# Kernel tuning notes

Measured on AMD Instinct MI355X. Metric: run time of the kernel, lower is better.

## Reference

```python
import jax, jax.numpy as jnp
import numpy as np
from jax import lax

B, L, D, DM, S, M, P = 8, 2048, 512, 1024, 32, 4, 4096


def setup_inputs() -> dict:
    key = jax.random.key(0)
    ks = jax.random.split(key, 13)
    emb = jax.random.normal(ks[0], (B, L, D), jnp.float32)
    pos = jax.random.randint(ks[1], (B, L), 1, P + 1)          # pos >= 1 (0 reserved for CLS)
    sid = jax.random.randint(ks[2], (B, L), 0, S)
    mod = jax.random.randint(ks[3], (B, L), 0, M)
    role = jax.random.randint(ks[4], (B, L), 0, 3)
    padding_mask = jax.random.uniform(ks[5], (B, L)) < 0.9
    W_proj = jax.random.normal(ks[6], (S, DM, D), jnp.float32) / np.float32(np.sqrt(D))
    b_proj = jax.random.normal(ks[7], (S, DM), jnp.float32) * 0.01
    cls_content = jax.random.normal(ks[8], (DM,), jnp.float32)
    pos_emb = jax.random.normal(ks[9], (P + 1, DM), jnp.float32) * 0.02
    id_emb = jax.random.normal(ks[10], (S + 1, DM), jnp.float32) * 0.02
    mod_emb = jax.random.normal(ks[11], (M, DM), jnp.float32) * 0.02
    role_emb = jax.random.normal(ks[12], (3, DM), jnp.float32) * 0.02
    return dict(emb=emb, pos=pos, sid=sid, mod=mod, role=role, padding_mask=padding_mask,
                W_proj=W_proj, b_proj=b_proj, cls_content=cls_content,
                pos_emb=pos_emb, id_emb=id_emb, mod_emb=mod_emb, role_emb=role_emb)


def _moe_project(emb, sid, padding_mask, W_proj, b_proj):
    """Per-token per-signal Linear: tokens[b,l] = W_proj[sid[b,l]] @ emb[b,l] + b_proj[sid[b,l]].
    Computed as S dense GEMMs masked per token (dense-dispatch MoE), avoiding an
    O(B*L*DM*D) gathered-weight tensor."""
    def step(acc, sWb):
        s, W, b = sWb
        y = jnp.einsum('bld,od->blo', emb, W) + b  # (B, L, DM)
        m = (sid == s) & padding_mask              # padded tokens stay zero
        return acc + jnp.where(m[..., None], y, 0.0), None
    acc0 = jnp.zeros(emb.shape[:2] + (W_proj.shape[1],), emb.dtype)
    acc, _ = lax.scan(step, acc0, (jnp.arange(W_proj.shape[0]), W_proj, b_proj))
    return acc


def reference(emb, pos, sid, mod, role, padding_mask,
              W_proj, b_proj, cls_content, pos_emb, id_emb, mod_emb, role_emb):
    Bc, Lc = pos.shape
    dm = cls_content.shape[0]
    cls_id = id_emb.shape[0] - 1  # == num_signals

    proj = _moe_project(emb, sid, padding_mask, W_proj, b_proj)  # (B, L, DM)

    cls = jnp.broadcast_to(cls_content, (Bc, 1, dm))
    tokens = jnp.concatenate([cls, proj], axis=1)                # (B, L+1, DM)

    pos_full = jnp.concatenate([jnp.zeros((Bc, 1), pos.dtype), pos], axis=1)
    sid_full = jnp.concatenate([jnp.full((Bc, 1), cls_id, sid.dtype), sid], axis=1)
    tokens = tokens + pos_emb[pos_full] + id_emb[sid_full]

    # modality + role embeddings only on non-CLS tokens (added even where padded, as in torch)
    tokens = tokens.at[:, 1:, :].add(mod_emb[mod] + role_emb[role])

    attn_keep = jnp.concatenate([jnp.ones((Bc, 1), bool), padding_mask], axis=1)
    return tokens, attn_keep
```

## Files before the change

### kernel.cpp

```cpp
#include <hip/hip_runtime.h>
#include <hip/hip_bf16.h>


#define NB   8
#define NL   2048
#define ND   512
#define NDM  1024
#define NS   32
#define NTOK (NB * NL)
#define LP1  (NL + 1)
#define MAXTILES 160
#define EXP_CAP 1024

static __device__ __forceinline__ size_t attn_off() { return (size_t)NB * LP1 * NDM; }

typedef __attribute__((ext_vector_type(8))) short bf16x8;
typedef __attribute__((ext_vector_type(4))) float f32x4;

__device__ __forceinline__ unsigned short f2bf(float f) {
    unsigned int x = __float_as_uint(f);
    x += 0x7fffu + ((x >> 16) & 1u);
    return (unsigned short)(x >> 16);
}

__device__ __forceinline__ float bf2f(unsigned short s) {
    return __uint_as_float(((unsigned int)s) << 16);
}

__device__ __forceinline__ bf16x8 cvt8(float4 a, float4 b) {
    bf16x8 r;
    r[0] = (short)__bfloat16_as_ushort(__float2bfloat16(a.x));
    r[1] = (short)__bfloat16_as_ushort(__float2bfloat16(a.y));
    r[2] = (short)__bfloat16_as_ushort(__float2bfloat16(a.z));
    r[3] = (short)__bfloat16_as_ushort(__float2bfloat16(a.w));
    r[4] = (short)__bfloat16_as_ushort(__float2bfloat16(b.x));
    r[5] = (short)__bfloat16_as_ushort(__float2bfloat16(b.y));
    r[6] = (short)__bfloat16_as_ushort(__float2bfloat16(b.z));
    r[7] = (short)__bfloat16_as_ushort(__float2bfloat16(b.w));
    return r;
}

__device__ __forceinline__ float4 ld4(const float* p) { return *(const float4*)p; }
__device__ __forceinline__ float4 add4(float4 a, float4 b) {
    return make_float4(a.x + b.x, a.y + b.y, a.z + b.z, a.w + b.w);
}

__global__ void k_bucket(const int* __restrict__ sid, const int* __restrict__ mask,
                         int* __restrict__ cnt, int* __restrict__ kidx,
                         int* __restrict__ tokList, float* __restrict__ out) {
    int t = blockIdx.x * 256 + threadIdx.x;
    if (t >= NTOK) return;
    int s = sid[t];
    bool keep = mask[t] != 0;
    int b = t >> 11, l = t & (NL - 1);
    out[attn_off() + (size_t)b * LP1 + l + 1] = keep ? 1.0f : 0.0f;
    if (t < NB) out[attn_off() + (size_t)t * LP1] = 1.0f;
    int ki = -1;
    if (keep) {
        ki = atomicAdd(&cnt[s], 1);
        if (ki < EXP_CAP) tokList[s * EXP_CAP + ki] = t;
    }
    kidx[t] = ki;
}

__global__ void k_tiles(const int* __restrict__ cnt, int* __restrict__ meta,
                        int* __restrict__ bOff, int4* __restrict__ tiles,
                        const float* __restrict__ me, const float* __restrict__ re,
                        float* __restrict__ mrT) {
    if (threadIdx.x == 0) {
        int idx = 0, cbase = 0;
        for (int e = 0; e < NS; ++e) {
            int c = min(cnt[e], EXP_CAP);
            bOff[e] = cbase;
            for (int r = 0; r < c; r += 128)
                tiles[idx++] = make_int4(e, r, min(128, c - r), cbase + r);
            cbase += c;
        }
        meta[0] = idx;
    }
    for (int i = threadIdx.x; i < 12 * (NDM / 4); i += 256) {
        int mr = i / (NDM / 4); int o = (i % (NDM / 4)) * 4;
        int m = mr / 3, ro = mr % 3;
        float4 v = add4(ld4(me + (size_t)m * NDM + o), ld4(re + (size_t)ro * NDM + o));
        *(float4*)&mrT[(size_t)mr * NDM + o] = v;
    }
}

__global__ __launch_bounds__(256, 4) void k_gemm(
    const float* __restrict__ emb, const float* __restrict__ Wp,
    const int* __restrict__ tokList, const int4* __restrict__ tiles,
    const int* __restrict__ meta, unsigned short* __restrict__ projC) {
    if (blockIdx.x >= meta[0]) return;
    int4 td = tiles[blockIdx.x];
    const int e = td.x, rowBase = td.y, nRows = td.z, cBase = td.w;
    const int nBase = blockIdx.y * 128;

    __shared__ short SA[128 * 32];
    __shared__ short SB[128 * 32];

    const int tid  = threadIdx.x;
    const int lane = tid & 63;
    const int w    = tid >> 6;
    const int wr   = w >> 1, wc = w & 1;
    const int fr   = lane & 15, kg = lane >> 4;

    const int srow = tid >> 2;
    const int sch  = tid & 3;
    const size_t eBase = (size_t)e * EXP_CAP + rowBase;
    int ar0 = (srow < nRows) ? srow : 0;
    int ar1 = (srow + 64 < nRows) ? srow + 64 : 0;
    int tok0 = tokList[eBase + ar0];
    int tok1 = tokList[eBase + ar1];
    const float* a0 = emb + (size_t)tok0 * ND + sch * 8;
    const float* a1 = emb + (size_t)tok1 * ND + sch * 8;
    const float* b0 = Wp + ((size_t)e * NDM + nBase + srow) * ND + sch * 8;
    const float* b1 = Wp + ((size_t)e * NDM + nBase + srow + 64) * ND + sch * 8;
    const int wo0 = srow * 32 + (sch ^ ((srow >> 1) & 3)) * 8;
    const int wo1 = wo0 + 64 * 32;

    f32x4 acc[4][4];
#pragma unroll
    for (int i = 0; i < 4; ++i)
#pragma unroll
        for (int j = 0; j < 4; ++j)
            acc[i][j] = (f32x4){0.f, 0.f, 0.f, 0.f};

    float4 ra0a = ld4(a0), ra0b = ld4(a0 + 4);
    float4 ra1a = ld4(a1), ra1b = ld4(a1 + 4);
    float4 rb0a = ld4(b0), rb0b = ld4(b0 + 4);
    float4 rb1a = ld4(b1), rb1b = ld4(b1 + 4);

    const int pc = kg ^ ((fr >> 1) & 3);
    for (int ks = 0; ks < ND / 32; ++ks) {
        __syncthreads();
        *(bf16x8*)&SA[wo0] = cvt8(ra0a, ra0b);
        *(bf16x8*)&SA[wo1] = cvt8(ra1a, ra1b);
        *(bf16x8*)&SB[wo0] = cvt8(rb0a, rb0b);
        *(bf16x8*)&SB[wo1] = cvt8(rb1a, rb1b);
        __syncthreads();
        if (ks < ND / 32 - 1) {
            const float* na0 = a0 + (ks + 1) * 32;
            const float* na1 = a1 + (ks + 1) * 32;
            const float* nb0 = b0 + (ks + 1) * 32;
            const float* nb1 = b1 + (ks + 1) * 32;
            ra0a = ld4(na0); ra0b = ld4(na0 + 4);
            ra1a = ld4(na1); ra1b = ld4(na1 + 4);
            rb0a = ld4(nb0); rb0b = ld4(nb0 + 4);
            rb1a = ld4(nb1); rb1b = ld4(nb1 + 4);
        }
        bf16x8 af[4], bv[4];
#pragma unroll
        for (int i = 0; i < 4; ++i)
            af[i] = *(const bf16x8*)&SA[(wr * 64 + i * 16 + fr) * 32 + pc * 8];
#pragma unroll
        for (int j = 0; j < 4; ++j)
            bv[j] = *(const bf16x8*)&SB[(wc * 64 + j * 16 + fr) * 32 + pc * 8];
#pragma unroll
        for (int i = 0; i < 4; ++i)
#pragma unroll
            for (int j = 0; j < 4; ++j)
                acc[i][j] = __builtin_amdgcn_mfma_f32_16x16x32_bf16(af[i], bv[j], acc[i][j], 0, 0, 0);
    }

#pragma unroll
    for (int i = 0; i < 4; ++i) {
#pragma unroll
        for (int r = 0; r < 4; ++r) {
            int row = wr * 64 + i * 16 + kg * 4 + r;
            if (row < nRows) {
                size_t crow = (size_t)(cBase + row) * NDM + nBase;
#pragma unroll
                for (int j = 0; j < 4; ++j)
                    projC[crow + wc * 64 + j * 16 + fr] = f2bf(acc[i][j][r]);
            }
        }
    }
}

__global__ void k_out(const int* __restrict__ pos, const int* __restrict__ sid,
                      const int* __restrict__ mod, const int* __restrict__ role,
                      const int* __restrict__ mask, const int* __restrict__ kidx,
                      const int* __restrict__ bOff,
                      const float* __restrict__ bp, const float* __restrict__ cls_c,
                      const float* __restrict__ pe, const float* __restrict__ ie,
                      const float* __restrict__ mrT,
                      const unsigned short* __restrict__ projC,
                      float* __restrict__ out) {
    int l1 = blockIdx.x;
    int b  = blockIdx.y;
    int o  = threadIdx.x * 4;
    float4 v;
    if (l1 == 0) {
        v = add4(add4(ld4(cls_c + o), ld4(pe + o)), ld4(ie + (size_t)NS * NDM + o));
    } else {
        int t = b * NL + l1 - 1;
        int p = pos[t], s = sid[t], mr = mod[t] * 3 + role[t];
        v = add4(ld4(pe + (size_t)p * NDM + o), ld4(ie + (size_t)s * NDM + o));
        v = add4(v, ld4(mrT + (size_t)mr * NDM + o));
        if (mask[t] != 0) {
            v = add4(v, ld4(bp + (size_t)s * NDM + o));
            int ki = kidx[t];
            if (ki >= 0 && ki < EXP_CAP) {
                const unsigned short* pr = projC + (size_t)(bOff[s] + ki) * NDM + o;
                v.x += bf2f(pr[0]); v.y += bf2f(pr[1]);
                v.z += bf2f(pr[2]); v.w += bf2f(pr[3]);
            }
        }
    }
    *(float4*)&out[((size_t)b * LP1 + l1) * NDM + o] = v;
}

extern "C" void kernel_launch(void* const* d_in, const int* in_sizes, int n_in,
                              void* d_out, int out_size, void* d_ws, size_t ws_size,
                              hipStream_t stream) {
    const float* emb  = (const float*)d_in[0];
    const int* pos    = (const int*)d_in[1];
    const int* sid    = (const int*)d_in[2];
    const int* mod    = (const int*)d_in[3];
    const int* role   = (const int*)d_in[4];
    const int* mask   = (const int*)d_in[5];
    const float* Wp   = (const float*)d_in[6];
    const float* bp   = (const float*)d_in[7];
    const float* cls  = (const float*)d_in[8];
    const float* pe   = (const float*)d_in[9];
    const float* ie   = (const float*)d_in[10];
    const float* me   = (const float*)d_in[11];
    const float* re   = (const float*)d_in[12];
    float* out = (float*)d_out;

    int* ws        = (int*)d_ws;
    int* cnt       = ws;
    int* meta      = ws + 32;
    int* bOff      = ws + 64;
    int4* tiles    = (int4*)(ws + 128);
    int* tokList   = ws + 1024;
    int* kidx      = ws + 33792;
    float* mrT     = (float*)(ws + 50176);
    unsigned short* projC = (unsigned short*)((char*)d_ws + 262144);

    hipMemsetAsync(ws, 0, 64 * sizeof(int), stream);
    k_bucket<<<NTOK / 256, 256, 0, stream>>>(sid, mask, cnt, kidx, tokList, out);
    k_tiles<<<1, 256, 0, stream>>>(cnt, meta, bOff, tiles, me, re, mrT);

    dim3 gg(MAXTILES, NDM / 128);
    k_gemm<<<gg, 256, 0, stream>>>(emb, Wp, tokList, tiles, meta, projC);

    dim3 go(LP1, NB);
    k_out<<<go, 256, 0, stream>>>(pos, sid, mod, role, mask, kidx, bOff,
                                  bp, cls, pe, ie, mrT, projC, out);
}
```

Measured before the change: 139.3 us.

## Double-buffer LDS tiles and prefetch two K-steps ahead in MoE GEMM

Converts the grouped GEMM's shared-memory staging to ping-pong buffers so each iteration needs one barrier instead of two. Global loads are issued two K-steps ahead and the bf16 conversion is deferred until after the MFMAs, so load latency overlaps with compute. It also drops the occupancy hint of 4 blocks per CU from launch bounds. The cost is doubled LDS use and more live registers, which may lower occupancy.

```diff
diff --git a/kernel.cpp b/kernel.cpp
--- a/kernel.cpp
+++ b/kernel.cpp
@@ -86,7 +86,7 @@
     }
 }
 
-__global__ __launch_bounds__(256, 4) void k_gemm(
+__global__ __launch_bounds__(256) void k_gemm(
     const float* __restrict__ emb, const float* __restrict__ Wp,
     const int* __restrict__ tokList, const int4* __restrict__ tiles,
     const int* __restrict__ meta, unsigned short* __restrict__ projC) {
@@ -95,8 +95,8 @@
     const int e = td.x, rowBase = td.y, nRows = td.z, cBase = td.w;
     const int nBase = blockIdx.y * 128;
 
-    __shared__ short SA[128 * 32];
-    __shared__ short SB[128 * 32];
+    __shared__ short SA[2][128 * 32];
+    __shared__ short SB[2][128 * 32];
 
     const int tid  = threadIdx.x;
     const int lane = tid & 63;
@@ -125,42 +125,54 @@
         for (int j = 0; j < 4; ++j)
             acc[i][j] = (f32x4){0.f, 0.f, 0.f, 0.f};
 
-    float4 ra0a = ld4(a0), ra0b = ld4(a0 + 4);
-    float4 ra1a = ld4(a1), ra1b = ld4(a1 + 4);
-    float4 rb0a = ld4(b0), rb0b = ld4(b0 + 4);
-    float4 rb1a = ld4(b1), rb1b = ld4(b1 + 4);
+    float4 ta0a, ta0b, ta1a, ta1b, tb0a, tb0b, tb1a, tb1b;
+    bf16x8 na0, na1, nb0, nb1;
+
+#define LDF(ks) do {                                           \
+        ta0a = ld4(a0 + (ks) * 32); ta0b = ld4(a0 + (ks) * 32 + 4); \
+        ta1a = ld4(a1 + (ks) * 32); ta1b = ld4(a1 + (ks) * 32 + 4); \
+        tb0a = ld4(b0 + (ks) * 32); tb0b = ld4(b0 + (ks) * 32 + 4); \
+        tb1a = ld4(b1 + (ks) * 32); tb1b = ld4(b1 + (ks) * 32 + 4); \
+    } while (0)
+#define CVT() do {                                             \
+        na0 = cvt8(ta0a, ta0b); na1 = cvt8(ta1a, ta1b);        \
+        nb0 = cvt8(tb0a, tb0b); nb1 = cvt8(tb1a, tb1b);        \
+    } while (0)
+
+    LDF(0); CVT();
+    *(bf16x8*)&SA[0][wo0] = na0;
+    *(bf16x8*)&SA[0][wo1] = na1;
+    *(bf16x8*)&SB[0][wo0] = nb0;
+    *(bf16x8*)&SB[0][wo1] = nb1;
+    LDF(1); CVT();
 
     const int pc = kg ^ ((fr >> 1) & 3);
     for (int ks = 0; ks < ND / 32; ++ks) {
-        __syncthreads();
-        *(bf16x8*)&SA[wo0] = cvt8(ra0a, ra0b);
-        *(bf16x8*)&SA[wo1] = cvt8(ra1a, ra1b);
-        *(bf16x8*)&SB[wo0] = cvt8(rb0a, rb0b);
-        *(bf16x8*)&SB[wo1] = cvt8(rb1a, rb1b);
+        const int cur = ks & 1;
         __syncthreads();
         if (ks < ND / 32 - 1) {
-            const float* na0 = a0 + (ks + 1) * 32;
-            const float* na1 = a1 + (ks + 1) * 32;
-            const float* nb0 = b0 + (ks + 1) * 32;
-            const float* nb1 = b1 + (ks + 1) * 32;
-            ra0a = ld4(na0); ra0b = ld4(na0 + 4);
-            ra1a = ld4(na1); ra1b = ld4(na1 + 4);
-            rb0a = ld4(nb0); rb0b = ld4(nb0 + 4);
-            rb1a = ld4(nb1); rb1b = ld4(nb1 + 4);
-        }
+            *(bf16x8*)&SA[cur ^ 1][wo0] = na0;
+            *(bf16x8*)&SA[cur ^ 1][wo1] = na1;
+            *(bf16x8*)&SB[cur ^ 1][wo0] = nb0;
+            *(bf16x8*)&SB[cur ^ 1][wo1] = nb1;
+        }
+        if (ks < ND / 32 - 2) LDF(ks + 2);
         bf16x8 af[4], bv[4];
 #pragma unroll
         for (int i = 0; i < 4; ++i)
-            af[i] = *(const bf16x8*)&SA[(wr * 64 + i * 16 + fr) * 32 + pc * 8];
+            af[i] = *(const bf16x8*)&SA[cur][(wr * 64 + i * 16 + fr) * 32 + pc * 8];
 #pragma unroll
         for (int j = 0; j < 4; ++j)
-            bv[j] = *(const bf16x8*)&SB[(wc * 64 + j * 16 + fr) * 32 + pc * 8];
+            bv[j] = *(const bf16x8*)&SB[cur][(wc * 64 + j * 16 + fr) * 32 + pc * 8];
 #pragma unroll
         for (int i = 0; i < 4; ++i)
 #pragma unroll
             for (int j = 0; j < 4; ++j)
                 acc[i][j] = __builtin_amdgcn_mfma_f32_16x16x32_bf16(af[i], bv[j], acc[i][j], 0, 0, 0);
-    }
+        if (ks < ND / 32 - 2) CVT();
+    }
+#undef LDF
+#undef CVT
 
 #pragma unroll
     for (int i = 0; i < 4; ++i) {
```

After: 136.6 us. Within noise of the previous version (-2.0%).
